# Kernel tuning notes

Hardware: AMD Instinct MI355X
Metric: run time of the kernel (lower is better)

## Reference

```python
import jax, jax.numpy as jnp
import numpy as np

T, H = 4096, 2048

def setup_inputs() -> dict:
    key = jax.random.key(0)
    k1, k2, k3 = jax.random.split(key, 3)
    x_sequence = jax.random.normal(k1, (T, H), dtype=jnp.float32)
    lamda = jax.random.normal(k2, (H,), dtype=jnp.float32) * 0.2
    B = jax.random.normal(k3, (H, H), dtype=jnp.float32) / jnp.sqrt(jnp.float32(H))
    return {"x_sequence": x_sequence, "lamda": lamda, "B": B}

def reference(x_sequence, lamda, B):
    # h_t = lamda \odot h_{t-1} + B @ x_t ; initial h_0 = 0 (reset_rtrl_state).
    # Returns stacked h over all T steps, matching torch.stack(outputs).
    def step(h, x_t):
        h_next = lamda * h + B @ x_t  # [H]
        return h_next, h_next
    h0 = jnp.zeros_like(lamda)
    _, hs = jax.lax.scan(step, h0, x_sequence)  # hs: [T, H]
    return hs
```

## Files before the change

### kernel.cpp

```cpp
#include <hip/hip_runtime.h>
#include <hip/hip_bf16.h>

#define T_DIM 4096
#define H_DIM 2048
#define K_DIM 2048
#define NCHUNK 64
#define CLEN 64
#define NT (K_DIM / 64)

typedef float f32x4 __attribute__((ext_vector_type(4)));
typedef _Float16 f16x8 __attribute__((ext_vector_type(8)));

typedef const __attribute__((address_space(1))) char* gp1;
typedef __attribute__((address_space(3))) char* lp3;

static const size_t nX = (size_t)T_DIM * K_DIM;
static const size_t nB = (size_t)H_DIM * K_DIM;

__global__ __launch_bounds__(256) void cvt_swz_all(const float* __restrict__ X,
                                                   const float* __restrict__ Bm,
                                                   _Float16* __restrict__ Xh,
                                                   _Float16* __restrict__ Bh) {
    size_t i = ((size_t)blockIdx.x * 256 + threadIdx.x) * 8;
    const float* in;
    _Float16* out;
    size_t j;
    if (i < nX) { in = X;  out = Xh; j = i; }
    else        { in = Bm; out = Bh; j = i - nX; }
    int row  = (int)(j >> 11);
    int colB = (int)(j & 2047) * 2;
    float a[8];
    *(f32x4*)(a)     = *(const f32x4*)(in + j);
    *(f32x4*)(a + 4) = *(const f32x4*)(in + j + 4);
    f16x8 h;
#pragma unroll
    for (int k = 0; k < 8; ++k) h[k] = (_Float16)a[k];
    size_t ob = (size_t)row * 4096 + (size_t)(colB ^ ((row & 7) << 4));
    *(f16x8*)((char*)out + ob) = h;
}

__global__ __launch_bounds__(512, 4) void gemm_f16(const _Float16* __restrict__ Xh,
                                                   const _Float16* __restrict__ Bh,
                                                   const float* __restrict__ lamda,
                                                   float* __restrict__ Y,
                                                   float* __restrict__ e) {
    __shared__ __align__(16) _Float16 sMem[2][2][128 * 64];

    int bid = blockIdx.x;
    int swz = (bid & 7) * 64 + (bid >> 3);
    const int h0 = (swz & 15) * 128;
    const int t0 = (swz >> 4) * 128;

    const int tid  = threadIdx.x;
    const int lane = tid & 63;
    const int wave = tid >> 6;
    const int wrow = (wave >> 2) & 1;
    const int wcol = (wave >> 1) & 1;
    const int kks  = wave & 1;
    const int ln15 = lane & 15;
    const int kq   = lane >> 4;

    f32x4 acc[4][4] = {};

    const int srow = tid >> 3;
    const int kcB  = (tid & 7) * 16;
    size_t gA0[2], gB0[2];
    unsigned ldsOff[2];
#pragma unroll
    for (int q = 0; q < 2; ++q) {
        gA0[q] = (size_t)(t0 + srow + q * 64) * 4096 + kcB;
        gB0[q] = (size_t)(h0 + srow + q * 64) * 4096 + kcB;
        ldsOff[q] = (unsigned)(q * 8192 + wave * 1024);
    }

    const int kb = kks * 64 + kq * 16;
    int offA[4], offB[4];
#pragma unroll
    for (int m = 0; m < 4; ++m) {
        int rA = wrow * 64 + m * 16 + ln15;
        offA[m] = rA * 128 + (kb ^ ((rA & 7) << 4));
        int rB = wcol * 64 + m * 16 + ln15;
        offB[m] = rB * 128 + (kb ^ ((rB & 7) << 4));
    }

#define STAGE(buf, kt)                                                                   \
    {                                                                                    \
        _Pragma("unroll")                                                                \
        for (int q = 0; q < 2; ++q) {                                                    \
            __builtin_amdgcn_global_load_lds((gp1)((const char*)Xh + gA0[q] + (kt) * 128), \
                                             (lp3)((char*)sMem[buf][0] + ldsOff[q]), 16, 0, 0); \
            __builtin_amdgcn_global_load_lds((gp1)((const char*)Bh + gB0[q] + (kt) * 128), \
                                             (lp3)((char*)sMem[buf][1] + ldsOff[q]), 16, 0, 0); \
        }                                                                                \
    }

#define COMPUTE(buf)                                                                     \
    {                                                                                    \
        const char* pA = (const char*)sMem[buf][0];                                      \
        const char* pB = (const char*)sMem[buf][1];                                      \
        f16x8 fa[4], fb[4];                                                              \
        _Pragma("unroll")                                                                \
        for (int m = 0; m < 4; ++m) fa[m] = *(const f16x8*)(pA + offA[m]);               \
        _Pragma("unroll")                                                                \
        for (int n = 0; n < 4; ++n) fb[n] = *(const f16x8*)(pB + offB[n]);               \
        _Pragma("unroll")                                                                \
        for (int m = 0; m < 4; ++m)                                                      \
            _Pragma("unroll")                                                            \
            for (int n = 0; n < 4; ++n)                                                  \
                acc[m][n] = __builtin_amdgcn_mfma_f32_16x16x32_f16(fa[m], fb[n],         \
                                                                  acc[m][n], 0, 0, 0);  \
    }

    STAGE(0, 0);
    __syncthreads();

    int cur = 0;
    for (int kt = 0; kt < NT; ++kt) {
        if (kt + 1 < NT) STAGE(cur ^ 1, kt + 1);
        COMPUTE(cur);
        __syncthreads();
        cur ^= 1;
    }
#undef STAGE
#undef COMPUTE

    const int p = wrow * 2 + wcol;
    float* red = (float*)sMem;
    if (kks == 1) {
#pragma unroll
        for (int m = 0; m < 4; ++m)
#pragma unroll
            for (int n = 0; n < 4; ++n)
                *(f32x4*)((char*)red + p * 16384 + (m * 4 + n) * 1024 + lane * 16) = acc[m][n];
    }
    __syncthreads();
    if (kks == 0) {
#pragma unroll
        for (int m = 0; m < 4; ++m)
#pragma unroll
            for (int n = 0; n < 4; ++n)
                acc[m][n] += *(const f32x4*)((const char*)red + p * 16384 + (m * 4 + n) * 1024 + lane * 16);

#pragma unroll
        for (int m = 0; m < 4; ++m) {
            int row = t0 + wrow * 64 + m * 16 + kq * 4;
#pragma unroll
            for (int n = 0; n < 4; ++n) {
                int col = h0 + wcol * 64 + n * 16 + ln15;
#pragma unroll
                for (int j = 0; j < 4; ++j)
                    Y[(size_t)(row + j) * H_DIM + col] = acc[m][n][j];
            }
        }

        const int c = (t0 >> 6) + wrow;
#pragma unroll
        for (int n = 0; n < 4; ++n) {
            int col = h0 + wcol * 64 + n * 16 + ln15;
            float lam  = lamda[col];
            float lam2 = lam * lam;
            float lam4 = lam2 * lam2;
            float lam16 = lam4 * lam4 * lam4 * lam4;
            float hsum = 0.f;
#pragma unroll
            for (int m = 0; m < 4; ++m) {
                float hm = fmaf(fmaf(fmaf(acc[m][n][0], lam, acc[m][n][1]), lam,
                                     acc[m][n][2]), lam, acc[m][n][3]);
                hsum = fmaf(hsum, lam16, hm);
            }
            float w = 1.f;
            if (kq < 3) w = lam4;
            if (kq < 2) w *= lam4;
            if (kq < 1) w *= lam4;
            float T = hsum * w;
            T += __shfl_xor(T, 16);
            T += __shfl_xor(T, 32);
            if (kq == 0) e[(size_t)c * H_DIM + col] = T;
        }
    }
}

__global__ __launch_bounds__(256) void scanCB(float* __restrict__ Y,
                                              const float* __restrict__ lamda,
                                              const float* __restrict__ e) {
    int c = blockIdx.x >> 3;
    int h = (blockIdx.x & 7) * 256 + threadIdx.x;
    float lam = lamda[h];
    float lamL = lam;
#pragma unroll
    for (int i = 0; i < 6; ++i) lamL *= lamL;
    float s = 0.f;
    for (int ci = 0; ci < c; ++ci)
        s = fmaf(lamL, s, e[(size_t)ci * H_DIM + h]);
    float* q = Y + (size_t)c * CLEN * H_DIM + h;
#pragma unroll
    for (int t = 0; t < CLEN; ++t) {
        float v = fmaf(lam, s, q[(size_t)t * H_DIM]);
        q[(size_t)t * H_DIM] = v;
        s = v;
    }
}

__global__ __launch_bounds__(256) void gemm_xbT_split(const float* __restrict__ X,
                                                      const float* __restrict__ Bm,
                                                      float* __restrict__ Y) {
    __shared__ __align__(16) _Float16 Ah[128 * 64];
    __shared__ __align__(16) _Float16 Al[128 * 64];
    __shared__ __align__(16) _Float16 Bh2[128 * 64];
    __shared__ __align__(16) _Float16 Bl[128 * 64];

    const int tid  = threadIdx.x;
    const int t0   = blockIdx.y * 128;
    const int h0   = blockIdx.x * 128;
    const int lane = tid & 63;
    const int wave = tid >> 6;
    const int wrow = wave >> 1;
    const int wcol = wave & 1;
    const int ln15 = lane & 15;
    const int kq   = lane >> 4;

    f32x4 acc[4][4] = {};

    int baseA[4], swzA[4], baseB[4], swzB[4];
#pragma unroll
    for (int m = 0; m < 4; ++m) {
        int rA = wrow * 64 + m * 16 + ln15;
        baseA[m] = rA * 128; swzA[m] = (rA & 7) << 4;
        int rB = wcol * 64 + m * 16 + ln15;
        baseB[m] = rB * 128; swzB[m] = (rB & 7) << 4;
    }

    for (int kt = 0; kt < NT; ++kt) {
        const int k0 = kt * 64;
        __syncthreads();
#pragma unroll
        for (int t = 0; t < 4; ++t) {
            int c   = tid + t * 256;
            int row = c >> 3;
            int kc  = (c & 7) * 8;
            size_t gA = (size_t)(t0 + row) * K_DIM + k0 + kc;
            size_t gB = (size_t)(h0 + row) * K_DIM + k0 + kc;
            float a[8], b[8];
            *(float4*)(a)     = *(const float4*)(X + gA);
            *(float4*)(a + 4) = *(const float4*)(X + gA + 4);
            *(float4*)(b)     = *(const float4*)(Bm + gB);
            *(float4*)(b + 4) = *(const float4*)(Bm + gB + 4);
            f16x8 ah, al, bh, bl;
#pragma unroll
            for (int j = 0; j < 8; ++j) {
                _Float16 hh = (_Float16)a[j];
                ah[j] = hh; al[j] = (_Float16)(a[j] - (float)hh);
                _Float16 gg = (_Float16)b[j];
                bh[j] = gg; bl[j] = (_Float16)(b[j] - (float)gg);
            }
            int off = row * 128 + ((kc * 2) ^ ((row & 7) << 4));
            *(f16x8*)((char*)Ah + off)  = ah;
            *(f16x8*)((char*)Al + off)  = al;
            *(f16x8*)((char*)Bh2 + off) = bh;
            *(f16x8*)((char*)Bl + off)  = bl;
        }
        __syncthreads();
#pragma unroll
        for (int kk = 0; kk < 2; ++kk) {
            const int kb = kk * 64 + kq * 16;
            f16x8 fa[4], fb[4], ft[4];
#pragma unroll
            for (int m = 0; m < 4; ++m)
                fa[m] = *(const f16x8*)((const char*)Ah + baseA[m] + (kb ^ swzA[m]));
#pragma unroll
            for (int m = 0; m < 4; ++m)
                fb[m] = *(const f16x8*)((const char*)Bh2 + baseB[m] + (kb ^ swzB[m]));
#pragma unroll
            for (int m = 0; m < 4; ++m)
#pragma unroll
                for (int n = 0; n < 4; ++n)
                    acc[m][n] = __builtin_amdgcn_mfma_f32_16x16x32_f16(fa[m], fb[n], acc[m][n], 0, 0, 0);
#pragma unroll
            for (int m = 0; m < 4; ++m)
                ft[m] = *(const f16x8*)((const char*)Bl + baseB[m] + (kb ^ swzB[m]));
#pragma unroll
            for (int m = 0; m < 4; ++m)
#pragma unroll
                for (int n = 0; n < 4; ++n)
                    acc[m][n] = __builtin_amdgcn_mfma_f32_16x16x32_f16(fa[m], ft[n], acc[m][n], 0, 0, 0);
#pragma unroll
            for (int m = 0; m < 4; ++m)
                ft[m] = *(const f16x8*)((const char*)Al + baseA[m] + (kb ^ swzA[m]));
#pragma unroll
            for (int m = 0; m < 4; ++m)
#pragma unroll
                for (int n = 0; n < 4; ++n)
                    acc[m][n] = __builtin_amdgcn_mfma_f32_16x16x32_f16(ft[m], fb[n], acc[m][n], 0, 0, 0);
        }
    }

#pragma unroll
    for (int m = 0; m < 4; ++m) {
        int row = t0 + wrow * 64 + m * 16 + kq * 4;
#pragma unroll
        for (int n = 0; n < 4; ++n) {
            int col = h0 + wcol * 64 + n * 16 + ln15;
#pragma unroll
            for (int j = 0; j < 4; ++j)
                Y[(size_t)(row + j) * H_DIM + col] = acc[m][n][j];
        }
    }
}

__global__ __launch_bounds__(256) void scanA(const float* __restrict__ Y,
                                             const float* __restrict__ lamda,
                                             float* __restrict__ e) {
    int c = blockIdx.x >> 3;
    int h = (blockIdx.x & 7) * 256 + threadIdx.x;
    float lam = lamda[h];
    float s = 0.f;
    const float* p = Y + (size_t)c * CLEN * H_DIM + h;
#pragma unroll
    for (int t = 0; t < CLEN; ++t) { s = fmaf(lam, s, *p); p += H_DIM; }
    e[(size_t)c * H_DIM + h] = s;
}

extern "C" void kernel_launch(void* const* d_in, const int* in_sizes, int n_in,
                              void* d_out, int out_size, void* d_ws, size_t ws_size,
                              hipStream_t stream) {
    const float* X   = (const float*)d_in[0];
    const float* lam = (const float*)d_in[1];
    const float* Bm  = (const float*)d_in[2];
    float* Y = (float*)d_out;

    const size_t needFused = (nX + nB) * sizeof(_Float16)
                           + (size_t)NCHUNK * H_DIM * sizeof(float);

    if (ws_size >= needFused) {
        _Float16* Xh = (_Float16*)d_ws;
        _Float16* Bh = Xh + nX;
        float* e = (float*)(Bh + nB);

        int cvtBlocks = (int)((nX + nB) / 8 / 256);
        cvt_swz_all<<<dim3(cvtBlocks), 256, 0, stream>>>(X, Bm, Xh, Bh);
        gemm_f16<<<dim3(512), 512, 0, stream>>>(Xh, Bh, lam, Y, e);
        scanCB<<<dim3(NCHUNK * 8), 256, 0, stream>>>(Y, lam, e);
    } else {
        dim3 grid(H_DIM / 128, T_DIM / 128);
        gemm_xbT_split<<<grid, 256, 0, stream>>>(X, Bm, Y);
        float* e = (float*)d_ws;
        scanA<<<dim3(NCHUNK * 8), 256, 0, stream>>>(Y, lam, e);
        scanCB<<<dim3(NCHUNK * 8), 256, 0, stream>>>(Y, lam, e);
    }
}
```

Baseline: 76.45 us.

## Fuse convert, GEMM and chunked scan into one cooperative kernel with grid syncs

Replaces the three-kernel path (fp16 convert, GEMM with chunk-end reduction, scan fixup) with a single cooperative kernel of 512 blocks. The blocks convert inputs, grid-sync, run the GEMM, write chunk carries, grid-sync again, then apply the cross-chunk carry to the accumulators still in registers. This avoids two kernel launches and the re-read and rewrite of the full output in the scan pass. The cost is two grid-wide barriers, a host occupancy query on every call, and a fallback to the old path if the cooperative launch fails. It also removes the split-precision fallback, so the function now returns without computing anything when the workspace is too small.

```diff
diff --git a/kernel.cpp b/kernel.cpp
--- a/kernel.cpp
+++ b/kernel.cpp
@@ -1,5 +1,6 @@
 #include <hip/hip_runtime.h>
 #include <hip/hip_bf16.h>
+#include <hip/hip_cooperative_groups.h>
 
 #define T_DIM 4096
 #define H_DIM 2048
@@ -8,6 +9,8 @@
 #define CLEN 64
 #define NT (K_DIM / 64)
 
+namespace cg = cooperative_groups;
+
 typedef float f32x4 __attribute__((ext_vector_type(4)));
 typedef _Float16 f16x8 __attribute__((ext_vector_type(8)));
 
@@ -16,6 +19,215 @@
 
 static const size_t nX = (size_t)T_DIM * K_DIM;
 static const size_t nB = (size_t)H_DIM * K_DIM;
+
+__global__ __launch_bounds__(512, 4) void fused_all(const float* __restrict__ X,
+                                                    const float* __restrict__ Bm,
+                                                    const float* __restrict__ lamda,
+                                                    float* __restrict__ Y,
+                                                    _Float16* __restrict__ Xh,
+                                                    _Float16* __restrict__ Bh,
+                                                    float* __restrict__ e) {
+    __shared__ __align__(16) _Float16 sMem[2][2][128 * 64];
+    cg::grid_group grid = cg::this_grid();
+
+    {
+        const size_t total = (nX + nB) / 8;
+        for (size_t it = (size_t)blockIdx.x * 512 + threadIdx.x; it < total;
+             it += (size_t)512 * 512) {
+            size_t i = it * 8;
+            const float* in; _Float16* out; size_t j;
+            if (i < nX) { in = X;  out = Xh; j = i; }
+            else        { in = Bm; out = Bh; j = i - nX; }
+            int row  = (int)(j >> 11);
+            int colB = (int)(j & 2047) * 2;
+            float a[8];
+            *(f32x4*)(a)     = *(const f32x4*)(in + j);
+            *(f32x4*)(a + 4) = *(const f32x4*)(in + j + 4);
+            f16x8 hv;
+#pragma unroll
+            for (int k2 = 0; k2 < 8; ++k2) hv[k2] = (_Float16)a[k2];
+            size_t ob = (size_t)row * 4096 + (size_t)(colB ^ ((row & 7) << 4));
+            *(f16x8*)((char*)out + ob) = hv;
+        }
+    }
+    __threadfence();
+    grid.sync();
+
+    int bid = blockIdx.x;
+    int swz = (bid & 7) * 64 + (bid >> 3);
+    const int h0 = (swz & 15) * 128;
+    const int t0 = (swz >> 4) * 128;
+
+    const int tid  = threadIdx.x;
+    const int lane = tid & 63;
+    const int wave = tid >> 6;
+    const int wrow = (wave >> 2) & 1;
+    const int wcol = (wave >> 1) & 1;
+    const int kks  = wave & 1;
+    const int ln15 = lane & 15;
+    const int kq   = lane >> 4;
+
+    f32x4 acc[4][4] = {};
+
+    {
+        const int srow = tid >> 3;
+        const int kcB  = (tid & 7) * 16;
+        size_t gA0[2], gB0[2];
+        unsigned ldsOff[2];
+#pragma unroll
+        for (int q = 0; q < 2; ++q) {
+            gA0[q] = (size_t)(t0 + srow + q * 64) * 4096 + kcB;
+            gB0[q] = (size_t)(h0 + srow + q * 64) * 4096 + kcB;
+            ldsOff[q] = (unsigned)(q * 8192 + wave * 1024);
+        }
+
+        const int kb = kks * 64 + kq * 16;
+        int offA[4], offB[4];
+#pragma unroll
+        for (int m = 0; m < 4; ++m) {
+            int rA = wrow * 64 + m * 16 + ln15;
+            offA[m] = rA * 128 + (kb ^ ((rA & 7) << 4));
+            int rB = wcol * 64 + m * 16 + ln15;
+            offB[m] = rB * 128 + (kb ^ ((rB & 7) << 4));
+        }
+
+#define STAGE(buf, kt)                                                                   \
+        {                                                                                \
+            _Pragma("unroll")                                                            \
+            for (int q = 0; q < 2; ++q) {                                                \
+                __builtin_amdgcn_global_load_lds((gp1)((const char*)Xh + gA0[q] + (kt) * 128), \
+                                                 (lp3)((char*)sMem[buf][0] + ldsOff[q]), 16, 0, 0); \
+                __builtin_amdgcn_global_load_lds((gp1)((const char*)Bh + gB0[q] + (kt) * 128), \
+                                                 (lp3)((char*)sMem[buf][1] + ldsOff[q]), 16, 0, 0); \
+            }                                                                            \
+        }
+
+#define COMPUTE(buf)                                                                     \
+        {                                                                                \
+            const char* pA = (const char*)sMem[buf][0];                                  \
+            const char* pB = (const char*)sMem[buf][1];                                  \
+            f16x8 fa[4], fb[4];                                                          \
+            _Pragma("unroll")                                                            \
+            for (int m = 0; m < 4; ++m) fa[m] = *(const f16x8*)(pA + offA[m]);           \
+            _Pragma("unroll")                                                            \
+            for (int n = 0; n < 4; ++n) fb[n] = *(const f16x8*)(pB + offB[n]);           \
+            _Pragma("unroll")                                                            \
+            for (int m = 0; m < 4; ++m)                                                  \
+                _Pragma("unroll")                                                        \
+                for (int n = 0; n < 4; ++n)                                              \
+                    acc[m][n] = __builtin_amdgcn_mfma_f32_16x16x32_f16(fa[m], fb[n],     \
+                                                                      acc[m][n], 0, 0, 0); \
+        }
+
+        STAGE(0, 0);
+        __syncthreads();
+        int cur = 0;
+        for (int kt = 0; kt < NT; ++kt) {
+            if (kt + 1 < NT) STAGE(cur ^ 1, kt + 1);
+            COMPUTE(cur);
+            __syncthreads();
+            cur ^= 1;
+        }
+#undef STAGE
+#undef COMPUTE
+    }
+
+    const int p = wrow * 2 + wcol;
+    float* red = (float*)sMem;
+    if (kks == 1) {
+#pragma unroll
+        for (int m = 0; m < 4; ++m)
+#pragma unroll
+            for (int n = 0; n < 4; ++n)
+                *(f32x4*)((char*)red + p * 16384 + (m * 4 + n) * 1024 + lane * 16) = acc[m][n];
+    }
+    __syncthreads();
+    const int c = (t0 >> 6) + wrow;
+    if (kks == 0) {
+#pragma unroll
+        for (int m = 0; m < 4; ++m)
+#pragma unroll
+            for (int n = 0; n < 4; ++n)
+                acc[m][n] += *(const f32x4*)((const char*)red + p * 16384 + (m * 4 + n) * 1024 + lane * 16);
+
+#pragma unroll
+        for (int n = 0; n < 4; ++n) {
+            int col = h0 + wcol * 64 + n * 16 + ln15;
+            float lam  = lamda[col];
+            float lam2 = lam * lam;
+            float lam4 = lam2 * lam2;
+            float lam16 = lam4 * lam4 * lam4 * lam4;
+            float hsum = 0.f;
+#pragma unroll
+            for (int m = 0; m < 4; ++m) {
+                float hm = fmaf(fmaf(fmaf(acc[m][n][0], lam, acc[m][n][1]), lam,
+                                     acc[m][n][2]), lam, acc[m][n][3]);
+                hsum = fmaf(hsum, lam16, hm);
+            }
+            float w = 1.f;
+            if (kq < 3) w = lam4;
+            if (kq < 2) w *= lam4;
+            if (kq < 1) w *= lam4;
+            float T = hsum * w;
+            T += __shfl_xor(T, 16);
+            T += __shfl_xor(T, 32);
+            if (kq == 0) e[(size_t)c * H_DIM + col] = T;
+        }
+    }
+    __threadfence();
+    grid.sync();
+
+    if (kks == 0) {
+#pragma unroll
+        for (int n = 0; n < 4; ++n) {
+            int col = h0 + wcol * 64 + n * 16 + ln15;
+            float lam   = lamda[col];
+            float lam2  = lam * lam;
+            float lam4  = lam2 * lam2;
+            float lam8  = lam4 * lam4;
+            float lam16 = lam8 * lam8;
+            float lam32 = lam16 * lam16;
+            float lamL  = lam32 * lam32;
+
+            float s = 0.f;
+            for (int ci = 0; ci < c; ++ci)
+                s = fmaf(lamL, s, e[(size_t)ci * H_DIM + col]);
+
+            float I[4], F[4];
+#pragma unroll
+            for (int m = 0; m < 4; ++m) {
+                float G = fmaf(fmaf(fmaf(acc[m][n][0], lam, acc[m][n][1]), lam,
+                                    acc[m][n][2]), lam, acc[m][n][3]);
+                float u1 = __shfl_up(G, 16);
+                float x  = (kq >= 1) ? fmaf(lam4, u1, G) : G;
+                float u2 = __shfl_up(x, 32);
+                x = (kq >= 2) ? fmaf(lam8, u2, x) : x;
+                I[m] = x;
+                F[m] = __shfl(x, 48 + ln15);
+            }
+
+            float lam4kq = 1.f;
+            if (kq >= 1) lam4kq = lam4;
+            if (kq >= 2) lam4kq *= lam4;
+            if (kq >= 3) lam4kq *= lam4;
+
+            float H = s;
+#pragma unroll
+            for (int m = 0; m < 4; ++m) {
+                float Iup = __shfl_up(I[m], 16);
+                float PRE = fmaf(lam4kq, H, (kq >= 1) ? Iup : 0.f);
+                int row = t0 + wrow * 64 + m * 16 + kq * 4;
+                float hh = PRE;
+#pragma unroll
+                for (int j = 0; j < 4; ++j) {
+                    hh = fmaf(lam, hh, acc[m][n][j]);
+                    Y[(size_t)(row + j) * H_DIM + col] = hh;
+                }
+                H = fmaf(lam16, H, F[m]);
+            }
+        }
+    }
+}
 
 __global__ __launch_bounds__(256) void cvt_swz_all(const float* __restrict__ X,
                                                    const float* __restrict__ Bm,
@@ -201,125 +413,6 @@
     }
 }
 
-__global__ __launch_bounds__(256) void gemm_xbT_split(const float* __restrict__ X,
-                                                      const float* __restrict__ Bm,
-                                                      float* __restrict__ Y) {
-    __shared__ __align__(16) _Float16 Ah[128 * 64];
-    __shared__ __align__(16) _Float16 Al[128 * 64];
-    __shared__ __align__(16) _Float16 Bh2[128 * 64];
-    __shared__ __align__(16) _Float16 Bl[128 * 64];
-
-    const int tid  = threadIdx.x;
-    const int t0   = blockIdx.y * 128;
-    const int h0   = blockIdx.x * 128;
-    const int lane = tid & 63;
-    const int wave = tid >> 6;
-    const int wrow = wave >> 1;
-    const int wcol = wave & 1;
-    const int ln15 = lane & 15;
-    const int kq   = lane >> 4;
-
-    f32x4 acc[4][4] = {};
-
-    int baseA[4], swzA[4], baseB[4], swzB[4];
-#pragma unroll
-    for (int m = 0; m < 4; ++m) {
-        int rA = wrow * 64 + m * 16 + ln15;
-        baseA[m] = rA * 128; swzA[m] = (rA & 7) << 4;
-        int rB = wcol * 64 + m * 16 + ln15;
-        baseB[m] = rB * 128; swzB[m] = (rB & 7) << 4;
-    }
-
-    for (int kt = 0; kt < NT; ++kt) {
-        const int k0 = kt * 64;
-        __syncthreads();
-#pragma unroll
-        for (int t = 0; t < 4; ++t) {
-            int c   = tid + t * 256;
-            int row = c >> 3;
-            int kc  = (c & 7) * 8;
-            size_t gA = (size_t)(t0 + row) * K_DIM + k0 + kc;
-            size_t gB = (size_t)(h0 + row) * K_DIM + k0 + kc;
-            float a[8], b[8];
-            *(float4*)(a)     = *(const float4*)(X + gA);
-            *(float4*)(a + 4) = *(const float4*)(X + gA + 4);
-            *(float4*)(b)     = *(const float4*)(Bm + gB);
-            *(float4*)(b + 4) = *(const float4*)(Bm + gB + 4);
-            f16x8 ah, al, bh, bl;
-#pragma unroll
-            for (int j = 0; j < 8; ++j) {
-                _Float16 hh = (_Float16)a[j];
-                ah[j] = hh; al[j] = (_Float16)(a[j] - (float)hh);
-                _Float16 gg = (_Float16)b[j];
-                bh[j] = gg; bl[j] = (_Float16)(b[j] - (float)gg);
-            }
-            int off = row * 128 + ((kc * 2) ^ ((row & 7) << 4));
-            *(f16x8*)((char*)Ah + off)  = ah;
-            *(f16x8*)((char*)Al + off)  = al;
-            *(f16x8*)((char*)Bh2 + off) = bh;
-            *(f16x8*)((char*)Bl + off)  = bl;
-        }
-        __syncthreads();
-#pragma unroll
-        for (int kk = 0; kk < 2; ++kk) {
-            const int kb = kk * 64 + kq * 16;
-            f16x8 fa[4], fb[4], ft[4];
-#pragma unroll
-            for (int m = 0; m < 4; ++m)
-                fa[m] = *(const f16x8*)((const char*)Ah + baseA[m] + (kb ^ swzA[m]));
-#pragma unroll
-            for (int m = 0; m < 4; ++m)
-                fb[m] = *(const f16x8*)((const char*)Bh2 + baseB[m] + (kb ^ swzB[m]));
-#pragma unroll
-            for (int m = 0; m < 4; ++m)
-#pragma unroll
-                for (int n = 0; n < 4; ++n)
-                    acc[m][n] = __builtin_amdgcn_mfma_f32_16x16x32_f16(fa[m], fb[n], acc[m][n], 0, 0, 0);
-#pragma unroll
-            for (int m = 0; m < 4; ++m)
-                ft[m] = *(const f16x8*)((const char*)Bl + baseB[m] + (kb ^ swzB[m]));
-#pragma unroll
-            for (int m = 0; m < 4; ++m)
-#pragma unroll
-                for (int n = 0; n < 4; ++n)
-                    acc[m][n] = __builtin_amdgcn_mfma_f32_16x16x32_f16(fa[m], ft[n], acc[m][n], 0, 0, 0);
-#pragma unroll
-            for (int m = 0; m < 4; ++m)
-                ft[m] = *(const f16x8*)((const char*)Al + baseA[m] + (kb ^ swzA[m]));
-#pragma unroll
-            for (int m = 0; m < 4; ++m)
-#pragma unroll
-                for (int n = 0; n < 4; ++n)
-                    acc[m][n] = __builtin_amdgcn_mfma_f32_16x16x32_f16(ft[m], fb[n], acc[m][n], 0, 0, 0);
-        }
-    }
-
-#pragma unroll
-    for (int m = 0; m < 4; ++m) {
-        int row = t0 + wrow * 64 + m * 16 + kq * 4;
-#pragma unroll
-        for (int n = 0; n < 4; ++n) {
-            int col = h0 + wcol * 64 + n * 16 + ln15;
-#pragma unroll
-            for (int j = 0; j < 4; ++j)
-                Y[(size_t)(row + j) * H_DIM + col] = acc[m][n][j];
-        }
-    }
-}
-
-__global__ __launch_bounds__(256) void scanA(const float* __restrict__ Y,
-                                             const float* __restrict__ lamda,
-                                             float* __restrict__ e) {
-    int c = blockIdx.x >> 3;
-    int h = (blockIdx.x & 7) * 256 + threadIdx.x;
-    float lam = lamda[h];
-    float s = 0.f;
-    const float* p = Y + (size_t)c * CLEN * H_DIM + h;
-#pragma unroll
-    for (int t = 0; t < CLEN; ++t) { s = fmaf(lam, s, *p); p += H_DIM; }
-    e[(size_t)c * H_DIM + h] = s;
-}
-
 extern "C" void kernel_launch(void* const* d_in, const int* in_sizes, int n_in,
                               void* d_out, int out_size, void* d_ws, size_t ws_size,
                               hipStream_t stream) {
@@ -331,20 +424,32 @@
     const size_t needFused = (nX + nB) * sizeof(_Float16)
                            + (size_t)NCHUNK * H_DIM * sizeof(float);
 
-    if (ws_size >= needFused) {
-        _Float16* Xh = (_Float16*)d_ws;
-        _Float16* Bh = Xh + nX;
-        float* e = (float*)(Bh + nB);
-
+    if (ws_size < needFused) {
+        return;
+    }
+
+    _Float16* Xh = (_Float16*)d_ws;
+    _Float16* Bh = Xh + nX;
+    float* e = (float*)(Bh + nB);
+
+    bool coopOK = false;
+    int maxB = 0;
+    if (hipOccupancyMaxActiveBlocksPerMultiprocessor(&maxB, fused_all, 512, 0)
+            == hipSuccess && maxB >= 2) {
+        const float *Xa = X, *Ba = Bm, *la = lam;
+        float *Ya = Y, *ea = e;
+        _Float16 *Xha = Xh, *Bha = Bh;
+        void* args[] = { (void*)&Xa, (void*)&Ba, (void*)&la, (void*)&Ya,
+                         (void*)&Xha, (void*)&Bha, (void*)&ea };
+        if (hipLaunchCooperativeKernel((const void*)fused_all, dim3(512),
+                                       dim3(512), args, 0, stream) == hipSuccess)
+            coopOK = true;
+    }
+
+    if (!coopOK) {
         int cvtBlocks = (int)((nX + nB) / 8 / 256);
         cvt_swz_all<<<dim3(cvtBlocks), 256, 0, stream>>>(X, Bm, Xh, Bh);
         gemm_f16<<<dim3(512), 512, 0, stream>>>(Xh, Bh, lam, Y, e);
         scanCB<<<dim3(NCHUNK * 8), 256, 0, stream>>>(Y, lam, e);
-    } else {
-        dim3 grid(H_DIM / 128, T_DIM / 128);
-        gemm_xbT_split<<<grid, 256, 0, stream>>>(X, Bm, Y);
-        float* e = (float*)d_ws;
-        scanA<<<dim3(NCHUNK * 8), 256, 0, stream>>>(Y, lam, e);
-        scanCB<<<dim3(NCHUNK * 8), 256, 0, stream>>>(Y, lam, e);
     }
 }
```

Result: no change. 76.42 us (-0.0%).
